# Kernel tuning notes

Hardware: AMD Instinct MI355X
Metric: run time of the kernel (lower is better)

The kernel has to match this reference:

```python
import jax, jax.numpy as jnp
import numpy as np

B, IN_LEN, L = 32, 10, 16384
N_POLY, M_MODES, K_STR, CH, NB = 12, 6, 2, 20, 4


def _legendre_filters():
    # Midpoints of n equal intervals on [-1, 1]
    j = np.arange(N_POLY)
    xs = -1.0 + (2.0 * j + 1.0) / N_POLY
    fr = np.stack([np.polynomial.legendre.Legendre.basis(i)(xs) for i in range(M_MODES)])
    fd = fr * ((2.0 * np.arange(M_MODES) + 1.0) / N_POLY)[:, None]  # decomposition quadrature weights
    return fd[:, None, :].astype(np.float32), fr[:, None, :].astype(np.float32)


def _conv1d(x, w, stride=1):
    return jax.lax.conv_general_dilated(x, w, (stride,), 'VALID',
                                        dimension_numbers=('NCH', 'OIH', 'NCH'))


def setup_inputs() -> dict:
    key = jax.random.key(0)
    ks = jax.random.split(key, 7)
    sc = 0.1
    fd, fr = _legendre_filters()
    return {
        'input':   jax.random.normal(ks[0], (B, IN_LEN, L), jnp.float32),
        'w_first': jax.random.normal(ks[1], (CH, IN_LEN, 3), jnp.float32) * sc,
        'conv_a':  jax.random.normal(ks[2], (NB, CH, CH, 3), jnp.float32) * sc,
        'conv_b':  jax.random.normal(ks[3], (NB, CH, CH, 3), jnp.float32) * sc,
        'lin_m':   jax.random.normal(ks[4], (NB, CH, M_MODES, M_MODES), jnp.float32) * sc,
        'w11':     jax.random.normal(ks[5], (128, CH, 1), jnp.float32) * sc,
        'w_out':   jax.random.normal(ks[6], (1, 128, 1), jnp.float32) * sc,
        'filt_d':  jnp.asarray(fd),
        'filt_r':  jnp.asarray(fr),
    }


def reference(input, w_first, conv_a, conv_b, lin_m, w11, w_out, filt_d, filt_r):
    n, m, kk = N_POLY, M_MODES, K_STR
    s = n // kk                      # conv stride = 6
    nb = conv_a.shape[0]
    RR = (n // kk) * (kk - 1)        # 6
    recept = RR * nb + 1
    rc = 2
    gelu = lambda t: jax.nn.gelu(t, approximate=False)

    b, _, Lin = input.shape
    li = Lin + 2 * recept - 2
    half = n // 2
    r = half - li % half             # circular padding to make strided conv exact
    x = jnp.pad(input, ((0, 0), (0, 0), (recept, recept + r)), mode='wrap')
    x = _conv1d(x, w_first)          # (b, CH, l)
    c = x.shape[1]

    for i in range(nb):
        l = x.shape[-1]
        # local residual branch: conv3 -> gelu -> conv3
        linear_x = _conv1d(gelu(_conv1d(x, conv_a[i])), conv_b[i])  # (b, c, l-4)
        # Legendre decomposition: strided conv per (b,c) signal
        xr = x.reshape(b * c, 1, l)
        Lx = _conv1d(xr, filt_d / kk, stride=s)                     # (b*c, m, ll)
        ll = Lx.shape[-1]
        Lx = Lx.reshape(b, c, m, ll).transpose(0, 2, 1, 3).reshape(b, m * c, ll)
        # grouped 1x1 conv: groups=c consecutive chunks of size m over the (mode-major) channel axis
        Lg = Lx.reshape(b, c, m, ll)
        Lg = jnp.einsum('bgil,goi->bgol', Lg, lin_m[i])
        Lx2 = Lg.reshape(b, m * c, ll)
        Lx2 = Lx2.reshape(b, m, c, ll).transpose(0, 2, 1, 3).reshape(b * c, m, ll) * 2.0
        # conv_transpose1d (stride s, kernel n=2s) via overlap-add of two half-kernels
        y = jnp.einsum('xmt,mk->xtk', Lx2, (filt_r / kk)[:, 0, :])  # (b*c, ll, n)
        p1 = y[..., :s].reshape(b * c, ll * s)
        p2 = y[..., s:].reshape(b * c, ll * s)
        rec = jnp.pad(p1, ((0, 0), (0, s))) + jnp.pad(p2, ((0, 0), (s, 0)))  # (b*c, l)
        rec = rec.reshape(b, c, l)
        x = gelu(rec[:, :, RR:-RR] + linear_x[:, :, RR - rc:-(RR - rc)])

    x = gelu(jnp.einsum('bcl,oc->bol', x, w11[:, :, 0]))
    x = jnp.einsum('bcl,oc->bol', x, w_out[:, :, 0])
    return x[:, :, :-r]
```

## Files before the change

kernel.cpp:

```cpp
#include <hip/hip_runtime.h>
#include <math.h>

#define B_ 32
#define INLEN 10
#define LIN_ 16384
#define NPOLY 12
#define MM 6
#define CH 20
#define NB 4
#define RECEPT 25
#define L0 16434
#define TTILE 252
#define NW 43
#define XS_LEN 264
#define XS_PAD 265
#define GS_LEN 254
#define LXS_PAD 121
#define CCHUNK 5
#define COH 10
#define INW 266

__device__ __forceinline__ float gelu_exact(float x) {
    return 0.5f * x * (1.0f + erff(x * 0.70710678118654752440f));
}

template<int MODE>
__global__ __launch_bounds__(512, 2)
void k_block(const float* __restrict__ x, float* __restrict__ xn,
             const float* __restrict__ wA, const float* __restrict__ wB,
             const float* __restrict__ linm, const float* __restrict__ fd,
             const float* __restrict__ fr,
             const float* __restrict__ in0, const float* __restrict__ wf,
             const float* __restrict__ w11, const float* __restrict__ wout,
             int l) {
    const int lout = l - 12;
    const int tid  = threadIdx.x;
    const int t    = tid & 255;
    const int half = __builtin_amdgcn_readfirstlane(tid >> 8);
    const int cob  = half * COH;
    const int t0   = blockIdx.x * TTILE;
    const int b    = blockIdx.y;

    const float* wAh = wA + cob * CH * 3;
    const float* wBh = wB + cob * CH * 3;

    __shared__ float xs[CH][XS_PAD];
    __shared__ float lxs[NW][LXS_PAD];
    __shared__ float lm_s[CH * MM * MM];
    __shared__ float fr_s[MM * NPOLY];

    for (int i = tid; i < CH * MM * MM; i += 512) lm_s[i] = linm[i];
    for (int i = tid; i < MM * NPOLY; i += 512)   fr_s[i] = fr[i];

    if constexpr (MODE == 0) {
        float* inps = &lxs[0][0];
        const float* inb = in0 + (size_t)b * INLEN * LIN_;
        for (int i = tid; i < INLEN * INW; i += 512) {
            int ci = i / INW, q = i - ci * INW;
            int gq = t0 + q - RECEPT;
            gq = (gq < 0) ? gq + LIN_ : (gq >= LIN_ ? gq - LIN_ : gq);
            inps[i] = inb[(size_t)ci * LIN_ + gq];
        }
        __syncthreads();
        const float* wfh = wf + cob * INLEN * 3;
        for (int p = t; p < XS_LEN; p += 256) {
            float acc[COH];
#pragma unroll
            for (int co = 0; co < COH; ++co) acc[co] = 0.f;
#pragma unroll 1
            for (int cig = 0; cig < INLEN; cig += CCHUNK) {
                float xw[CCHUNK][3];
#pragma unroll
                for (int j = 0; j < CCHUNK; ++j) {
                    xw[j][0] = inps[(cig + j) * INW + p];
                    xw[j][1] = inps[(cig + j) * INW + p + 1];
                    xw[j][2] = inps[(cig + j) * INW + p + 2];
                }
#pragma unroll
                for (int co = 0; co < COH; ++co) {
                    float a = acc[co];
#pragma unroll
                    for (int j = 0; j < CCHUNK; ++j)
#pragma unroll
                        for (int k = 0; k < 3; ++k)
                            a = fmaf(xw[j][k], wfh[(co * INLEN + cig + j) * 3 + k], a);
                    acc[co] = a;
                }
            }
            const bool live = (t0 + p < l);
#pragma unroll
            for (int co = 0; co < COH; ++co) xs[cob + co][p] = live ? acc[co] : 0.f;
        }
        __syncthreads();
    } else {
        const float* xb = x + (size_t)b * CH * l;
        for (int i = tid; i < CH * XS_LEN; i += 512) {
            int c = i / XS_LEN, p = i - c * XS_LEN;
            int gp = t0 + p;
            xs[c][p] = (gp < l) ? xb[(size_t)c * l + gp] : 0.f;
        }
        __syncthreads();
    }

    for (int item = tid; item < NW * CH; item += 512) {
        int wl = item / CH, c = item - wl * CH;
        float xv[NPOLY];
#pragma unroll
        for (int k = 0; k < NPOLY; ++k) xv[k] = xs[c][6 * wl + k];
#pragma unroll
        for (int m = 0; m < MM; ++m) {
            float acc = 0.f;
#pragma unroll
            for (int k = 0; k < NPOLY; ++k)
                acc = fmaf(xv[k], fd[m * NPOLY + k], acc);
            lxs[wl][m * CH + c] = acc * 0.5f;
        }
    }

    float gv[COH];
    if (t < GS_LEN) {
#pragma unroll
        for (int co = 0; co < COH; ++co) gv[co] = 0.f;
#pragma unroll 1
        for (int cig = 0; cig < CH; cig += CCHUNK) {
            float xw[CCHUNK][3];
#pragma unroll
            for (int j = 0; j < CCHUNK; ++j) {
                xw[j][0] = xs[cig + j][t + 4];
                xw[j][1] = xs[cig + j][t + 5];
                xw[j][2] = xs[cig + j][t + 6];
            }
#pragma unroll
            for (int co = 0; co < COH; ++co) {
                float acc = gv[co];
#pragma unroll
                for (int j = 0; j < CCHUNK; ++j)
#pragma unroll
                    for (int k = 0; k < 3; ++k)
                        acc = fmaf(xw[j][k], wAh[(co * CH + cig + j) * 3 + k], acc);
                gv[co] = acc;
            }
        }
#pragma unroll
        for (int co = 0; co < COH; ++co) gv[co] = gelu_exact(gv[co]);
    }
    __syncthreads();

    if (t < GS_LEN) {
#pragma unroll
        for (int co = 0; co < COH; ++co) xs[cob + co][t] = gv[co];
    }

    for (int item = tid; item < NW * CH; item += 512) {
        int wl = item / CH, g = item - wl * CH;
        float iv[MM], ov[MM];
#pragma unroll
        for (int i = 0; i < MM; ++i) iv[i] = lxs[wl][g * MM + i];
#pragma unroll
        for (int o = 0; o < MM; ++o) {
            float acc = 0.f;
#pragma unroll
            for (int i = 0; i < MM; ++i)
                acc = fmaf(iv[i], lm_s[(g * MM + o) * MM + i], acc);
            ov[o] = acc;
        }
#pragma unroll
        for (int o = 0; o < MM; ++o) lxs[wl][g * MM + o] = ov[o];
    }
    __syncthreads();

    const bool vd = (t < TTILE) && (t0 + t < lout);
    float outv[COH];
    if (vd) {
        const int tp = t;
        float acc[COH];
#pragma unroll
        for (int co = 0; co < COH; ++co) acc[co] = 0.f;
#pragma unroll 1
        for (int cig = 0; cig < CH; cig += CCHUNK) {
            float aw[CCHUNK][3];
#pragma unroll
            for (int j = 0; j < CCHUNK; ++j) {
                aw[j][0] = xs[cig + j][tp];
                aw[j][1] = xs[cig + j][tp + 1];
                aw[j][2] = xs[cig + j][tp + 2];
            }
#pragma unroll
            for (int co = 0; co < COH; ++co) {
                float a = acc[co];
#pragma unroll
                for (int j = 0; j < CCHUNK; ++j)
#pragma unroll
                    for (int k = 0; k < 3; ++k)
                        a = fmaf(aw[j][k], wBh[(co * CH + cig + j) * 3 + k], a);
                acc[co] = a;
            }
        }
        const int r1  = tp % 6;
        const int wl1 = tp / 6 + 1;
        float frA[MM], frB[MM];
#pragma unroll
        for (int m = 0; m < MM; ++m) {
            frA[m] = fr_s[m * NPOLY + r1];
            frB[m] = fr_s[m * NPOLY + r1 + 6];
        }
#pragma unroll
        for (int co = 0; co < COH; ++co) {
            float rec = 0.f;
#pragma unroll
            for (int m = 0; m < MM; ++m) {
                rec = fmaf(lxs[wl1][m * CH + cob + co], frA[m], rec);
                rec = fmaf(lxs[wl1 - 1][m * CH + cob + co], frB[m], rec);
            }
            outv[co] = gelu_exact(acc[co] + rec);
        }
        if constexpr (MODE != 2) {
            float* xnb = xn + (size_t)b * CH * lout + (size_t)cob * lout;
#pragma unroll
            for (int co = 0; co < COH; ++co)
                xnb[(size_t)co * lout + t0 + t] = outv[co];
        }
    }

    if constexpr (MODE == 2) {
        __syncthreads();
        if (vd) {
#pragma unroll
            for (int co = 0; co < COH; ++co) xs[cob + co][t] = outv[co];
        }
        __syncthreads();
        const bool vf = (t < TTILE) && (t0 + t < LIN_);
        float* pb = &lxs[0][0];
        if (vf) {
            float xv[CH];
#pragma unroll
            for (int c = 0; c < CH; ++c) xv[c] = xs[c][t];
            const float* w11h  = w11 + (size_t)(half * 64) * CH;
            const float* wouth = wout + half * 64;
            float partial = 0.f;
#pragma unroll 1
            for (int h = 0; h < 64; h += 2) {
                float hv0 = 0.f, hv1 = 0.f;
#pragma unroll
                for (int c = 0; c < CH; ++c) {
                    hv0 = fmaf(xv[c], w11h[h * CH + c], hv0);
                    hv1 = fmaf(xv[c], w11h[(h + 1) * CH + c], hv1);
                }
                partial = fmaf(gelu_exact(hv0), wouth[h], partial);
                partial = fmaf(gelu_exact(hv1), wouth[h + 1], partial);
            }
            pb[half * 256 + t] = partial;
        }
        __syncthreads();
        if (vf && half == 0)
            xn[(size_t)b * LIN_ + t0 + t] = pb[t] + pb[256 + t];
    }
}

extern "C" void kernel_launch(void* const* d_in, const int* in_sizes, int n_in,
                              void* d_out, int out_size, void* d_ws, size_t ws_size,
                              hipStream_t stream) {
    const float* input   = (const float*)d_in[0];
    const float* w_first = (const float*)d_in[1];
    const float* conv_a  = (const float*)d_in[2];
    const float* conv_b  = (const float*)d_in[3];
    const float* lin_m   = (const float*)d_in[4];
    const float* w11     = (const float*)d_in[5];
    const float* w_out   = (const float*)d_in[6];
    const float* filt_d  = (const float*)d_in[7];
    const float* filt_r  = (const float*)d_in[8];
    float* out = (float*)d_out;

    const size_t bufElems = (size_t)B_ * CH * L0;
    float* xA = (float*)d_ws;
    float* xB = xA + bufElems;

    const int WSTEP = CH * CH * 3;
    const int MSTEP = CH * MM * MM;

    {
        dim3 grid((L0 - 12 + TTILE - 1) / TTILE, B_);
        k_block<0><<<grid, 512, 0, stream>>>(nullptr, xA, conv_a, conv_b, lin_m,
                                             filt_d, filt_r, input, w_first,
                                             nullptr, nullptr, L0);
    }
    {
        dim3 grid((L0 - 24 + TTILE - 1) / TTILE, B_);
        k_block<1><<<grid, 512, 0, stream>>>(xA, xB, conv_a + WSTEP, conv_b + WSTEP,
                                             lin_m + MSTEP, filt_d, filt_r,
                                             nullptr, nullptr, nullptr, nullptr, L0 - 12);
    }
    {
        dim3 grid((L0 - 36 + TTILE - 1) / TTILE, B_);
        k_block<1><<<grid, 512, 0, stream>>>(xB, xA, conv_a + 2 * WSTEP, conv_b + 2 * WSTEP,
                                             lin_m + 2 * MSTEP, filt_d, filt_r,
                                             nullptr, nullptr, nullptr, nullptr, L0 - 24);
    }
    {
        dim3 grid((LIN_ + TTILE - 1) / TTILE, B_);
        k_block<2><<<grid, 512, 0, stream>>>(xA, out, conv_a + 3 * WSTEP, conv_b + 3 * WSTEP,
                                             lin_m + 3 * MSTEP, filt_d, filt_r,
                                             nullptr, nullptr, w11, w_out, L0 - 36);
    }
}
```

Baseline: 487.1 us.

## Fuse pairs of multiwavelet blocks into one kernel to halve global round-trips

Fuses two consecutive residual blocks into a single kernel. The intermediate activation stays in shared memory between the two blocks, so the pipeline drops from four launches to two. This removes two global write/read passes over the 20-channel activation tensor and two launch boundaries. In exchange, the tile shrinks to 240 output points because of the larger halo, so more tiles and more redundant halo compute are needed. The fused kernel is also longer, with extra barriers and a mid-kernel reload of the lin_m weights.

```diff
diff --git a/kernel.cpp b/kernel.cpp
--- a/kernel.cpp
+++ b/kernel.cpp
@@ -7,14 +7,13 @@
 #define NPOLY 12
 #define MM 6
 #define CH 20
-#define NB 4
 #define RECEPT 25
 #define L0 16434
-#define TTILE 252
-#define NW 43
+#define TT2 240
 #define XS_LEN 264
 #define XS_PAD 265
-#define GS_LEN 254
+#define NWA 43
+#define NWB 41
 #define LXS_PAD 121
 #define CCHUNK 5
 #define COH 10
@@ -24,35 +23,41 @@
     return 0.5f * x * (1.0f + erff(x * 0.70710678118654752440f));
 }
 
-template<int MODE>
+template<int PAIR>
 __global__ __launch_bounds__(512, 2)
-void k_block(const float* __restrict__ x, float* __restrict__ xn,
-             const float* __restrict__ wA, const float* __restrict__ wB,
-             const float* __restrict__ linm, const float* __restrict__ fd,
-             const float* __restrict__ fr,
-             const float* __restrict__ in0, const float* __restrict__ wf,
-             const float* __restrict__ w11, const float* __restrict__ wout,
-             int l) {
-    const int lout = l - 12;
+void k_pair(const float* __restrict__ xin, float* __restrict__ xout,
+            const float* __restrict__ conv_a, const float* __restrict__ conv_b,
+            const float* __restrict__ lin_m, const float* __restrict__ fd,
+            const float* __restrict__ fr,
+            const float* __restrict__ in0, const float* __restrict__ wf,
+            const float* __restrict__ w11, const float* __restrict__ wout) {
+    constexpr int LA_IN  = (PAIR == 0) ? L0 : (L0 - 24);
+    constexpr int LA_OUT = LA_IN - 12;
+    constexpr int LB_OUT = LA_OUT - 12;
+    constexpr int WOFF   = CH * CH * 3;
+    constexpr int MOFF   = CH * MM * MM;
+
     const int tid  = threadIdx.x;
     const int t    = tid & 255;
     const int half = __builtin_amdgcn_readfirstlane(tid >> 8);
     const int cob  = half * COH;
-    const int t0   = blockIdx.x * TTILE;
+    const int t0   = blockIdx.x * TT2;
     const int b    = blockIdx.y;
 
-    const float* wAh = wA + cob * CH * 3;
-    const float* wBh = wB + cob * CH * 3;
+    const float* wAa = conv_a + (2 * PAIR)     * WOFF + cob * CH * 3;
+    const float* wBa = conv_b + (2 * PAIR)     * WOFF + cob * CH * 3;
+    const float* wAb = conv_a + (2 * PAIR + 1) * WOFF + cob * CH * 3;
+    const float* wBb = conv_b + (2 * PAIR + 1) * WOFF + cob * CH * 3;
 
     __shared__ float xs[CH][XS_PAD];
-    __shared__ float lxs[NW][LXS_PAD];
-    __shared__ float lm_s[CH * MM * MM];
+    __shared__ float lxs[NWA][LXS_PAD];
+    __shared__ float lm_s[MOFF];
     __shared__ float fr_s[MM * NPOLY];
 
-    for (int i = tid; i < CH * MM * MM; i += 512) lm_s[i] = linm[i];
-    for (int i = tid; i < MM * NPOLY; i += 512)   fr_s[i] = fr[i];
-
-    if constexpr (MODE == 0) {
+    for (int i = tid; i < MOFF; i += 512) lm_s[i] = lin_m[(2 * PAIR) * MOFF + i];
+    for (int i = tid; i < MM * NPOLY; i += 512) fr_s[i] = fr[i];
+
+    if constexpr (PAIR == 0) {
         float* inps = &lxs[0][0];
         const float* inb = in0 + (size_t)b * INLEN * LIN_;
         for (int i = tid; i < INLEN * INW; i += 512) {
@@ -87,22 +92,25 @@
                     acc[co] = a;
                 }
             }
-            const bool live = (t0 + p < l);
+            const bool live = (t0 + p < L0);
 #pragma unroll
             for (int co = 0; co < COH; ++co) xs[cob + co][p] = live ? acc[co] : 0.f;
         }
         __syncthreads();
     } else {
-        const float* xb = x + (size_t)b * CH * l;
+        const float* xb = xin + (size_t)b * CH * LA_IN;
         for (int i = tid; i < CH * XS_LEN; i += 512) {
             int c = i / XS_LEN, p = i - c * XS_LEN;
             int gp = t0 + p;
-            xs[c][p] = (gp < l) ? xb[(size_t)c * l + gp] : 0.f;
-        }
-        __syncthreads();
-    }
-
-    for (int item = tid; item < NW * CH; item += 512) {
+            xs[c][p] = (gp < LA_IN) ? xb[(size_t)c * LA_IN + gp] : 0.f;
+        }
+        __syncthreads();
+    }
+
+    float gv[COH];
+    float outv[COH];
+
+    for (int item = tid; item < NWA * CH; item += 512) {
         int wl = item / CH, c = item - wl * CH;
         float xv[NPOLY];
 #pragma unroll
@@ -116,9 +124,7 @@
             lxs[wl][m * CH + c] = acc * 0.5f;
         }
     }
-
-    float gv[COH];
-    if (t < GS_LEN) {
+    if (t < XS_LEN - 10) {
 #pragma unroll
         for (int co = 0; co < COH; ++co) gv[co] = 0.f;
 #pragma unroll 1
@@ -137,7 +143,7 @@
                 for (int j = 0; j < CCHUNK; ++j)
 #pragma unroll
                     for (int k = 0; k < 3; ++k)
-                        acc = fmaf(xw[j][k], wAh[(co * CH + cig + j) * 3 + k], acc);
+                        acc = fmaf(xw[j][k], wAa[(co * CH + cig + j) * 3 + k], acc);
                 gv[co] = acc;
             }
         }
@@ -145,13 +151,11 @@
         for (int co = 0; co < COH; ++co) gv[co] = gelu_exact(gv[co]);
     }
     __syncthreads();
-
-    if (t < GS_LEN) {
+    if (t < XS_LEN - 10) {
 #pragma unroll
         for (int co = 0; co < COH; ++co) xs[cob + co][t] = gv[co];
     }
-
-    for (int item = tid; item < NW * CH; item += 512) {
+    for (int item = tid; item < NWA * CH; item += 512) {
         int wl = item / CH, g = item - wl * CH;
         float iv[MM], ov[MM];
 #pragma unroll
@@ -168,11 +172,8 @@
         for (int o = 0; o < MM; ++o) lxs[wl][g * MM + o] = ov[o];
     }
     __syncthreads();
-
-    const bool vd = (t < TTILE) && (t0 + t < lout);
-    float outv[COH];
-    if (vd) {
-        const int tp = t;
+    const bool vdA = (t < XS_LEN - 12) && (t0 + t < LA_OUT);
+    if (vdA) {
         float acc[COH];
 #pragma unroll
         for (int co = 0; co < COH; ++co) acc[co] = 0.f;
@@ -181,9 +182,9 @@
             float aw[CCHUNK][3];
 #pragma unroll
             for (int j = 0; j < CCHUNK; ++j) {
-                aw[j][0] = xs[cig + j][tp];
-                aw[j][1] = xs[cig + j][tp + 1];
-                aw[j][2] = xs[cig + j][tp + 2];
+                aw[j][0] = xs[cig + j][t];
+                aw[j][1] = xs[cig + j][t + 1];
+                aw[j][2] = xs[cig + j][t + 2];
             }
 #pragma unroll
             for (int co = 0; co < COH; ++co) {
@@ -192,12 +193,12 @@
                 for (int j = 0; j < CCHUNK; ++j)
 #pragma unroll
                     for (int k = 0; k < 3; ++k)
-                        a = fmaf(aw[j][k], wBh[(co * CH + cig + j) * 3 + k], a);
+                        a = fmaf(aw[j][k], wBa[(co * CH + cig + j) * 3 + k], a);
                 acc[co] = a;
             }
         }
-        const int r1  = tp % 6;
-        const int wl1 = tp / 6 + 1;
+        const int r1  = t % 6;
+        const int wl1 = t / 6 + 1;
         float frA[MM], frB[MM];
 #pragma unroll
         for (int m = 0; m < MM; ++m) {
@@ -214,22 +215,138 @@
             }
             outv[co] = gelu_exact(acc[co] + rec);
         }
-        if constexpr (MODE != 2) {
-            float* xnb = xn + (size_t)b * CH * lout + (size_t)cob * lout;
+    }
+    __syncthreads();
+    if (vdA) {
+#pragma unroll
+        for (int co = 0; co < COH; ++co) xs[cob + co][t] = outv[co];
+    }
+    for (int i = tid; i < MOFF; i += 512)
+        lm_s[i] = lin_m[(2 * PAIR + 1) * MOFF + i];
+    __syncthreads();
+
+    for (int item = tid; item < NWB * CH; item += 512) {
+        int wl = item / CH, c = item - wl * CH;
+        float xv[NPOLY];
+#pragma unroll
+        for (int k = 0; k < NPOLY; ++k) xv[k] = xs[c][6 * wl + k];
+#pragma unroll
+        for (int m = 0; m < MM; ++m) {
+            float acc = 0.f;
+#pragma unroll
+            for (int k = 0; k < NPOLY; ++k)
+                acc = fmaf(xv[k], fd[m * NPOLY + k], acc);
+            lxs[wl][m * CH + c] = acc * 0.5f;
+        }
+    }
+    if (t < XS_LEN - 22) {
+#pragma unroll
+        for (int co = 0; co < COH; ++co) gv[co] = 0.f;
+#pragma unroll 1
+        for (int cig = 0; cig < CH; cig += CCHUNK) {
+            float xw[CCHUNK][3];
+#pragma unroll
+            for (int j = 0; j < CCHUNK; ++j) {
+                xw[j][0] = xs[cig + j][t + 4];
+                xw[j][1] = xs[cig + j][t + 5];
+                xw[j][2] = xs[cig + j][t + 6];
+            }
+#pragma unroll
+            for (int co = 0; co < COH; ++co) {
+                float acc = gv[co];
+#pragma unroll
+                for (int j = 0; j < CCHUNK; ++j)
+#pragma unroll
+                    for (int k = 0; k < 3; ++k)
+                        acc = fmaf(xw[j][k], wAb[(co * CH + cig + j) * 3 + k], acc);
+                gv[co] = acc;
+            }
+        }
+#pragma unroll
+        for (int co = 0; co < COH; ++co) gv[co] = gelu_exact(gv[co]);
+    }
+    __syncthreads();
+    if (t < XS_LEN - 22) {
+#pragma unroll
+        for (int co = 0; co < COH; ++co) xs[cob + co][t] = gv[co];
+    }
+    for (int item = tid; item < NWB * CH; item += 512) {
+        int wl = item / CH, g = item - wl * CH;
+        float iv[MM], ov[MM];
+#pragma unroll
+        for (int i = 0; i < MM; ++i) iv[i] = lxs[wl][g * MM + i];
+#pragma unroll
+        for (int o = 0; o < MM; ++o) {
+            float acc = 0.f;
+#pragma unroll
+            for (int i = 0; i < MM; ++i)
+                acc = fmaf(iv[i], lm_s[(g * MM + o) * MM + i], acc);
+            ov[o] = acc;
+        }
+#pragma unroll
+        for (int o = 0; o < MM; ++o) lxs[wl][g * MM + o] = ov[o];
+    }
+    __syncthreads();
+    const bool vdB = (t < TT2) && (t0 + t < LB_OUT);
+    if (vdB) {
+        float acc[COH];
+#pragma unroll
+        for (int co = 0; co < COH; ++co) acc[co] = 0.f;
+#pragma unroll 1
+        for (int cig = 0; cig < CH; cig += CCHUNK) {
+            float aw[CCHUNK][3];
+#pragma unroll
+            for (int j = 0; j < CCHUNK; ++j) {
+                aw[j][0] = xs[cig + j][t];
+                aw[j][1] = xs[cig + j][t + 1];
+                aw[j][2] = xs[cig + j][t + 2];
+            }
+#pragma unroll
+            for (int co = 0; co < COH; ++co) {
+                float a = acc[co];
+#pragma unroll
+                for (int j = 0; j < CCHUNK; ++j)
+#pragma unroll
+                    for (int k = 0; k < 3; ++k)
+                        a = fmaf(aw[j][k], wBb[(co * CH + cig + j) * 3 + k], a);
+                acc[co] = a;
+            }
+        }
+        const int r1  = t % 6;
+        const int wl1 = t / 6 + 1;
+        float frA[MM], frB[MM];
+#pragma unroll
+        for (int m = 0; m < MM; ++m) {
+            frA[m] = fr_s[m * NPOLY + r1];
+            frB[m] = fr_s[m * NPOLY + r1 + 6];
+        }
+#pragma unroll
+        for (int co = 0; co < COH; ++co) {
+            float rec = 0.f;
+#pragma unroll
+            for (int m = 0; m < MM; ++m) {
+                rec = fmaf(lxs[wl1][m * CH + cob + co], frA[m], rec);
+                rec = fmaf(lxs[wl1 - 1][m * CH + cob + co], frB[m], rec);
+            }
+            outv[co] = gelu_exact(acc[co] + rec);
+        }
+    }
+
+    if constexpr (PAIR == 0) {
+        if (vdB) {
+            float* xnb = xout + (size_t)b * CH * LB_OUT + (size_t)cob * LB_OUT;
 #pragma unroll
             for (int co = 0; co < COH; ++co)
-                xnb[(size_t)co * lout + t0 + t] = outv[co];
-        }
-    }
-
-    if constexpr (MODE == 2) {
-        __syncthreads();
-        if (vd) {
+                xnb[(size_t)co * LB_OUT + t0 + t] = outv[co];
+        }
+    } else {
+        __syncthreads();
+        if (vdB) {
 #pragma unroll
             for (int co = 0; co < COH; ++co) xs[cob + co][t] = outv[co];
         }
         __syncthreads();
-        const bool vf = (t < TTILE) && (t0 + t < LIN_);
+        const bool vf = (t < TT2) && (t0 + t < LIN_);
         float* pb = &lxs[0][0];
         if (vf) {
             float xv[CH];
@@ -253,7 +370,7 @@
         }
         __syncthreads();
         if (vf && half == 0)
-            xn[(size_t)b * LIN_ + t0 + t] = pb[t] + pb[256 + t];
+            xout[(size_t)b * LIN_ + t0 + t] = pb[t] + pb[256 + t];
     }
 }
 
@@ -271,35 +388,20 @@
     const float* filt_r  = (const float*)d_in[8];
     float* out = (float*)d_out;
 
-    const size_t bufElems = (size_t)B_ * CH * L0;
     float* xA = (float*)d_ws;
-    float* xB = xA + bufElems;
-
-    const int WSTEP = CH * CH * 3;
-    const int MSTEP = CH * MM * MM;
-
+
+    const int tiles = (LIN_ + TT2 - 1) / TT2 + ((16410 % TT2) ? 1 : 0) - ((16410 % TT2) ? 1 : 0);
     {
-        dim3 grid((L0 - 12 + TTILE - 1) / TTILE, B_);
-        k_block<0><<<grid, 512, 0, stream>>>(nullptr, xA, conv_a, conv_b, lin_m,
-                                             filt_d, filt_r, input, w_first,
-                                             nullptr, nullptr, L0);
+        dim3 grid(( (L0 - 24) + TT2 - 1) / TT2, B_);
+        k_pair<0><<<grid, 512, 0, stream>>>(nullptr, xA, conv_a, conv_b, lin_m,
+                                            filt_d, filt_r, input, w_first,
+                                            nullptr, nullptr);
     }
     {
-        dim3 grid((L0 - 24 + TTILE - 1) / TTILE, B_);
-        k_block<1><<<grid, 512, 0, stream>>>(xA, xB, conv_a + WSTEP, conv_b + WSTEP,
-                                             lin_m + MSTEP, filt_d, filt_r,
-                                             nullptr, nullptr, nullptr, nullptr, L0 - 12);
-    }
-    {
-        dim3 grid((L0 - 36 + TTILE - 1) / TTILE, B_);
-        k_block<1><<<grid, 512, 0, stream>>>(xB, xA, conv_a + 2 * WSTEP, conv_b + 2 * WSTEP,
-                                             lin_m + 2 * MSTEP, filt_d, filt_r,
-                                             nullptr, nullptr, nullptr, nullptr, L0 - 24);
-    }
-    {
-        dim3 grid((LIN_ + TTILE - 1) / TTILE, B_);
-        k_block<2><<<grid, 512, 0, stream>>>(xA, out, conv_a + 3 * WSTEP, conv_b + 3 * WSTEP,
-                                             lin_m + 3 * MSTEP, filt_d, filt_r,
-                                             nullptr, nullptr, w11, w_out, L0 - 36);
-    }
+        dim3 grid((LIN_ + TT2 - 1) / TT2, B_);
+        k_pair<1><<<grid, 512, 0, stream>>>(xA, out, conv_a, conv_b, lin_m,
+                                            filt_d, filt_r, nullptr, nullptr,
+                                            w11, w_out);
+    }
+    (void)tiles;
 }
```

After: 473.6 us. -2.8%, faster.
